# Optimization experiments

Measured on AMD Instinct MI355X. Metric: run time of the kernel, lower is better.

The kernel has to match this reference:

```python
import jax, jax.numpy as jnp
import numpy as np

B, C, N = 8, 768, 256
H = 12            # num_heads[0]
D = C // H        # head_dim = 64


def setup_inputs() -> dict:
    key = jax.random.key(0)
    ks = jax.random.split(key, 4)
    s = 0.02
    return {
        "x_ori": jax.random.normal(ks[0], (B, C, N), jnp.float32),
        "cross": jax.random.normal(ks[1], (B, C, N), jnp.float32),
        "W_proj": jax.random.normal(ks[2], (C, C), jnp.float32) * s,
        "b_proj": jnp.zeros((C,), jnp.float32),
        "W_dep": jax.random.normal(ks[3], (C, C), jnp.float32) * s,
        "b_dep": jnp.zeros((C,), jnp.float32),
    }


def reference(x_ori, cross, W_proj, b_proj, W_dep, b_dep):
    # x_ori, cross: [B, C, N] with channel axis factored as (head_dim D, num_heads H)
    Bn, Cn, Nn = x_ori.shape
    Nc = cross.shape[-1]
    scale = D ** (-0.5)

    # 'B (d H) N -> B d (H N)'
    x = x_ori.reshape(Bn, D, H, Nn).reshape(Bn, D, H * Nn)

    # proj over channel axis (1x1 conv): [B, C, Nc]
    cp = jnp.einsum('oc,bcn->bon', W_proj, cross) + b_proj[None, :, None]
    cp = cp.reshape(Bn, D, H, Nc).reshape(Bn, D, H * Nc)      # 'B (d H) Nc -> B d (H Nc)'

    # 'B (d H) Nc -> B (H Nc) d'
    cr = cross.reshape(Bn, D, H, Nc).transpose(0, 2, 3, 1).reshape(Bn, H * Nc, D)

    # raw attention (no softmax in original source)
    atten = jnp.einsum('bdm,bdn->bmn', x, cp) * scale          # [B, H*N, H*Nc]
    out = jnp.einsum('bmn,bnd->bmd', atten, cr)                # [B, H*N, D]

    # 'B (N H) d -> B N (H d)'  (note (num, head) grouping per source)
    out = out.reshape(Bn, Nn, H, D).reshape(Bn, Nn, H * D)

    y = out @ W_dep.T + b_dep                                  # deproj: [B, N, C]
    # skip connection (dropout is identity at eval / drop_ratio=0)
    return x_ori + y.transpose(0, 2, 1)
```

## Files before the change

### kernel.cpp

```cpp
#include <hip/hip_runtime.h>

typedef unsigned short u16;
typedef short bf16x8 __attribute__((ext_vector_type(8)));
typedef float f32x4 __attribute__((ext_vector_type(4)));

#define BB 8
#define CC 768
#define NN 256
#define HH 12
#define DD 64
#define BCN 196608
#define SCALE 0.125f
#define LDP 72

__device__ __forceinline__ u16 f2b(float f) {
    union { float f; unsigned int i; } v; v.f = f;
    unsigned int r = v.i + 0x7FFFu + ((v.i >> 16) & 1u);
    return (u16)(r >> 16);
}

#define MFMA8(ASP, BSP, ACC)                                                              \
    _Pragma("unroll")                                                                     \
    for (int kk = 0; kk < 2; ++kk) {                                                      \
        bf16x8 a0 = *reinterpret_cast<bf16x8*>((ASP) + (wm + tx) * LDP + kk * 32 + q * 8);\
        bf16x8 a1 = *reinterpret_cast<bf16x8*>((ASP) + (wm + 16 + tx) * LDP + kk * 32 + q * 8);\
        bf16x8 b0 = *reinterpret_cast<bf16x8*>((BSP) + (wn + tx) * LDP + kk * 32 + q * 8);\
        bf16x8 b1 = *reinterpret_cast<bf16x8*>((BSP) + (wn + 16 + tx) * LDP + kk * 32 + q * 8);\
        ACC[0][0] = __builtin_amdgcn_mfma_f32_16x16x32_bf16(a0, b0, ACC[0][0], 0, 0, 0);  \
        ACC[0][1] = __builtin_amdgcn_mfma_f32_16x16x32_bf16(a0, b1, ACC[0][1], 0, 0, 0);  \
        ACC[1][0] = __builtin_amdgcn_mfma_f32_16x16x32_bf16(a1, b0, ACC[1][0], 0, 0, 0);  \
        ACC[1][1] = __builtin_amdgcn_mfma_f32_16x16x32_bf16(a1, b1, ACC[1][1], 0, 0, 0);  \
    }

__global__ __launch_bounds__(256) void k_pg(
    const float* __restrict__ Wp, const float* __restrict__ cross,
    const float* __restrict__ bp, float* __restrict__ G)
{
    __shared__ __align__(16) u16 As[64 * LDP];
    __shared__ __align__(16) u16 Bs[64 * LDP];
    __shared__ __align__(16) float T[64][68];
    const int h  = blockIdx.x;
    const int n0 = blockIdx.y * 64;
    const int b  = blockIdx.z;
    const int t = threadIdx.x;
    const int lane = t & 63, wave = t >> 6;
    const int q = lane >> 4, tx = lane & 15;
    const int wm = (wave & 1) * 32, wn = (wave >> 1) * 32;
    const int r4 = t >> 2, cq = t & 3;
    const float* crb = cross + b * BCN;
    const float* wrow = Wp + (r4 * HH + h) * CC;

    f32x4 acc[2][2] = {};
    float4 ra[4], rc[4];
    #pragma unroll
    for (int u = 0; u < 4; ++u) {
        const int cl = (cq + 4 * u) * 4;
        ra[u] = *reinterpret_cast<const float4*>(wrow + cl);
        rc[u] = *reinterpret_cast<const float4*>(crb + r4 * NN + n0 + cl);
    }
    for (int it = 0; it < 12; ++it) {
        if (it > 0) __syncthreads();
        {
            u16* dstA = As + r4 * LDP;
            #pragma unroll
            for (int u = 0; u < 4; ++u) {
                const int cl = (cq + 4 * u) * 4;
                ushort4 w; w.x = f2b(ra[u].x); w.y = f2b(ra[u].y);
                w.z = f2b(ra[u].z); w.w = f2b(ra[u].w);
                *reinterpret_cast<ushort4*>(dstA + cl) = w;
                T[r4][cl + 0] = rc[u].x; T[r4][cl + 1] = rc[u].y;
                T[r4][cl + 2] = rc[u].z; T[r4][cl + 3] = rc[u].w;
            }
        }
        if (it < 11) {
            const int c0 = (it + 1) * 64;
            #pragma unroll
            for (int u = 0; u < 4; ++u) {
                const int cl = (cq + 4 * u) * 4;
                ra[u] = *reinterpret_cast<const float4*>(wrow + c0 + cl);
                rc[u] = *reinterpret_cast<const float4*>(crb + (c0 + r4) * NN + n0 + cl);
            }
        }
        __syncthreads();
        {
            const int nn = t >> 2, dq = t & 3;
            u16* dst = Bs + nn * LDP;
            #pragma unroll
            for (int u = 0; u < 4; ++u) {
                const int c4 = (dq + 4 * u) * 4;
                ushort4 w;
                w.x = f2b(T[c4 + 0][nn]); w.y = f2b(T[c4 + 1][nn]);
                w.z = f2b(T[c4 + 2][nn]); w.w = f2b(T[c4 + 3][nn]);
                *reinterpret_cast<ushort4*>(dst + c4) = w;
            }
        }
        __syncthreads();
        MFMA8(As, Bs, acc)
    }
    __syncthreads();
    float4 rg[4];
    #pragma unroll
    for (int u = 0; u < 4; ++u)
        rg[u] = *reinterpret_cast<const float4*>(crb + (r4 * HH + h) * NN + n0 + (cq + 4 * u) * 4);
    #pragma unroll
    for (int i = 0; i < 2; ++i)
        #pragma unroll
        for (int r = 0; r < 4; ++r) {
            const int ddl = wm + i * 16 + q * 4 + r;
            const float bias = bp[ddl * HH + h];
            #pragma unroll
            for (int j = 0; j < 2; ++j)
                As[ddl * LDP + wn + j * 16 + tx] = f2b(acc[i][j][r] + bias);
        }
    {
        u16* dst = Bs + r4 * LDP;
        #pragma unroll
        for (int u = 0; u < 4; ++u) {
            const int cl = (cq + 4 * u) * 4;
            ushort4 w; w.x = f2b(rg[u].x); w.y = f2b(rg[u].y);
            w.z = f2b(rg[u].z); w.w = f2b(rg[u].w);
            *reinterpret_cast<ushort4*>(dst + cl) = w;
        }
    }
    __syncthreads();
    f32x4 g[2][2] = {};
    MFMA8(As, Bs, g)
    float* Gb = G + b * 4096;
    #pragma unroll
    for (int i = 0; i < 2; ++i)
        #pragma unroll
        for (int j = 0; j < 2; ++j)
            #pragma unroll
            for (int r = 0; r < 4; ++r) {
                const int dd = wm + i * 16 + q * 4 + r;
                const int dc = wn + j * 16 + tx;
                atomicAdd(Gb + dc * DD + dd, g[i][j][r] * SCALE);
            }
}

__global__ __launch_bounds__(256) void k_xm(
    const float* __restrict__ x, const float* __restrict__ G, u16* __restrict__ U)
{
    __shared__ __align__(16) u16 As[64 * LDP];
    __shared__ __align__(16) u16 Bs[64 * LDP];
    __shared__ __align__(16) float T[64][68];
    const int m0 = blockIdx.x * 64;
    const int b  = blockIdx.y;
    const int h   = m0 >> 8;
    const int nn0 = m0 & 255;
    const int t = threadIdx.x;
    const int lane = t & 63, wave = t >> 6;
    const int q = lane >> 4, tx = lane & 15;
    const int wm = (wave & 1) * 32, wn = (wave >> 1) * 32;
    const float* xb = x + b * BCN;
    const float* Gb = G + b * 4096;
    f32x4 acc[2][2] = {};
    {
        const int d = t >> 2, fq = t & 3;
        const float* src = xb + (d * HH + h) * NN + nn0;
        #pragma unroll
        for (int u = 0; u < 4; ++u) {
            const int nl = (fq + 4 * u) * 4;
            float4 v = *reinterpret_cast<const float4*>(src + nl);
            T[d][nl + 0] = v.x; T[d][nl + 1] = v.y; T[d][nl + 2] = v.z; T[d][nl + 3] = v.w;
        }
    }
    {
        const int r = t >> 2, cq = t & 3;
        const float* src = Gb + r * DD;
        u16* dst = Bs + r * LDP;
        #pragma unroll
        for (int u = 0; u < 4; ++u) {
            const int cl = (cq + 4 * u) * 4;
            float4 v = *reinterpret_cast<const float4*>(src + cl);
            ushort4 w; w.x = f2b(v.x); w.y = f2b(v.y); w.z = f2b(v.z); w.w = f2b(v.w);
            *reinterpret_cast<ushort4*>(dst + cl) = w;
        }
    }
    __syncthreads();
    {
        const int nn = t >> 2, dq = t & 3;
        u16* dst = As + nn * LDP;
        #pragma unroll
        for (int u = 0; u < 4; ++u) {
            const int d4 = (dq + 4 * u) * 4;
            ushort4 w;
            w.x = f2b(T[d4 + 0][nn]); w.y = f2b(T[d4 + 1][nn]);
            w.z = f2b(T[d4 + 2][nn]); w.w = f2b(T[d4 + 3][nn]);
            *reinterpret_cast<ushort4*>(dst + d4) = w;
        }
    }
    __syncthreads();
    MFMA8(As, Bs, acc)
    u16* Ub = U + b * BCN;
    #pragma unroll
    for (int i = 0; i < 2; ++i)
        #pragma unroll
        for (int j = 0; j < 2; ++j)
            #pragma unroll
            for (int r = 0; r < 4; ++r) {
                const int m  = m0 + wm + i * 16 + q * 4 + r;
                const int dd = wn + j * 16 + tx;
                Ub[m * DD + dd] = f2b(acc[i][j][r]);
            }
}

__global__ __launch_bounds__(256) void k_dep(
    const float* __restrict__ Wd, const u16* __restrict__ U,
    const float* __restrict__ bd, const float* __restrict__ x, float* __restrict__ out)
{
    __shared__ __align__(16) u16 As[2][64 * LDP];
    __shared__ __align__(16) u16 Bs[2][64 * LDP];
    const int n0 = blockIdx.x * 64;
    const int o0 = blockIdx.y * 64;
    const int b  = blockIdx.z;
    const int t = threadIdx.x;
    const int lane = t & 63, wave = t >> 6;
    const int q = lane >> 4, tx = lane & 15;
    const int wm = (wave & 1) * 32, wn = (wave >> 1) * 32;
    const int r4 = t >> 2, cq = t & 3;
    const int r8 = t >> 3, ch = (t & 7) * 8;
    const u16* Ub = U + b * BCN;
    float4 ra[4]; uint4 rb[2];

    auto loadit = [&](int it) {
        const int c0 = it * 64;
        const float* srcA = Wd + (o0 + r4) * CC + c0;
        #pragma unroll
        for (int u = 0; u < 4; ++u)
            ra[u] = *reinterpret_cast<const float4*>(srcA + (cq + 4 * u) * 4);
        rb[0] = *reinterpret_cast<const uint4*>(Ub + (n0 + r8) * CC + c0 + ch);
        rb[1] = *reinterpret_cast<const uint4*>(Ub + (n0 + r8 + 32) * CC + c0 + ch);
    };
    auto storeit = [&](int buf) {
        u16* dst = As[buf] + r4 * LDP;
        #pragma unroll
        for (int u = 0; u < 4; ++u) {
            const int cl = (cq + 4 * u) * 4;
            ushort4 w; w.x = f2b(ra[u].x); w.y = f2b(ra[u].y);
            w.z = f2b(ra[u].z); w.w = f2b(ra[u].w);
            *reinterpret_cast<ushort4*>(dst + cl) = w;
        }
        *reinterpret_cast<uint4*>(Bs[buf] + r8 * LDP + ch) = rb[0];
        *reinterpret_cast<uint4*>(Bs[buf] + (r8 + 32) * LDP + ch) = rb[1];
    };

    f32x4 acc[2][2] = {};
    loadit(0);
    storeit(0);
    #pragma unroll 2
    for (int it = 0; it < 12; ++it) {
        const int cur = it & 1;
        if (it < 11) loadit(it + 1);
        __syncthreads();
        MFMA8(As[cur], Bs[cur], acc)
        if (it < 11) storeit(cur ^ 1);
    }
    #pragma unroll
    for (int i = 0; i < 2; ++i)
        #pragma unroll
        for (int j = 0; j < 2; ++j)
            #pragma unroll
            for (int r = 0; r < 4; ++r) {
                const int o = o0 + wm + i * 16 + q * 4 + r;
                const int n = n0 + wn + j * 16 + tx;
                const int idx = b * BCN + o * NN + n;
                out[idx] = acc[i][j][r] + bd[o] + x[idx];
            }
}

extern "C" void kernel_launch(void* const* d_in, const int* in_sizes, int n_in,
                              void* d_out, int out_size, void* d_ws, size_t ws_size,
                              hipStream_t stream) {
    const float* x_ori = (const float*)d_in[0];
    const float* cross = (const float*)d_in[1];
    const float* Wp    = (const float*)d_in[2];
    const float* bp    = (const float*)d_in[3];
    const float* Wd    = (const float*)d_in[4];
    const float* bd    = (const float*)d_in[5];
    float* out = (float*)d_out;

    u16*   U  = (u16*)d_ws;
    float* G  = (float*)((char*)d_ws + (size_t)BB * BCN * sizeof(u16));

    hipMemsetAsync(G, 0, (size_t)BB * DD * DD * sizeof(float), stream);
    k_pg <<<dim3(HH, 4, BB), 256, 0, stream>>>(Wp, cross, bp, G);
    k_xm <<<dim3(48, BB), 256, 0, stream>>>(x_ori, G, U);
    k_dep<<<dim3(4, 12, BB), 256, 0, stream>>>(Wd, U, bd, x_ori, out);
}
```

Baseline: 133.3 us.

## Fuse three kernels and memset into one cooperative kernel with grid syncs

Merges the projection/Gram, x-times-G, and deprojection kernels, plus the G zeroing memset, into a single cooperative launch of 384 blocks separated by grid-wide barriers. Shared memory is aliased across the phases. The aim is to remove the memset and the separate kernel launch gaps. In exchange it adds three grid.sync barriers and the overhead of a cooperative launch, and the grid must fit on the device all at once.

```diff
diff --git a/kernel.cpp b/kernel.cpp
--- a/kernel.cpp
+++ b/kernel.cpp
@@ -1,4 +1,7 @@
 #include <hip/hip_runtime.h>
+#include <hip/hip_cooperative_groups.h>
+
+namespace cg = cooperative_groups;
 
 typedef unsigned short u16;
 typedef short bf16x8 __attribute__((ext_vector_type(8)));
@@ -12,6 +15,7 @@
 #define BCN 196608
 #define SCALE 0.125f
 #define LDP 72
+#define BUFB 9216
 
 __device__ __forceinline__ u16 f2b(float f) {
     union { float f; unsigned int i; } v; v.f = f;
@@ -32,241 +36,248 @@
         ACC[1][1] = __builtin_amdgcn_mfma_f32_16x16x32_bf16(a1, b1, ACC[1][1], 0, 0, 0);  \
     }
 
-__global__ __launch_bounds__(256) void k_pg(
+__global__ __launch_bounds__(256, 2) void k_all(
     const float* __restrict__ Wp, const float* __restrict__ cross,
-    const float* __restrict__ bp, float* __restrict__ G)
+    const float* __restrict__ bp, const float* __restrict__ x,
+    const float* __restrict__ Wd, const float* __restrict__ bd,
+    u16* __restrict__ U, float* __restrict__ G, float* __restrict__ out)
 {
-    __shared__ __align__(16) u16 As[64 * LDP];
-    __shared__ __align__(16) u16 Bs[64 * LDP];
-    __shared__ __align__(16) float T[64][68];
-    const int h  = blockIdx.x;
-    const int n0 = blockIdx.y * 64;
-    const int b  = blockIdx.z;
+    __shared__ __align__(16) unsigned char smem[4 * BUFB];
+    cg::grid_group grid = cg::this_grid();
+
+    const int bid = blockIdx.x;
     const int t = threadIdx.x;
     const int lane = t & 63, wave = t >> 6;
     const int q = lane >> 4, tx = lane & 15;
     const int wm = (wave & 1) * 32, wn = (wave >> 1) * 32;
     const int r4 = t >> 2, cq = t & 3;
-    const float* crb = cross + b * BCN;
-    const float* wrow = Wp + (r4 * HH + h) * CC;
-
-    f32x4 acc[2][2] = {};
-    float4 ra[4], rc[4];
-    #pragma unroll
-    for (int u = 0; u < 4; ++u) {
-        const int cl = (cq + 4 * u) * 4;
-        ra[u] = *reinterpret_cast<const float4*>(wrow + cl);
-        rc[u] = *reinterpret_cast<const float4*>(crb + r4 * NN + n0 + cl);
-    }
-    for (int it = 0; it < 12; ++it) {
-        if (it > 0) __syncthreads();
+    const int b = bid / 48;
+
+    if ((bid % 48) == 0) {
+        float4 z = {0.f, 0.f, 0.f, 0.f};
+        float* Gb = G + b * 4096;
+        #pragma unroll
+        for (int j = 0; j < 4; ++j)
+            *reinterpret_cast<float4*>(Gb + t * 4 + j * 1024) = z;
+    }
+
+    {
+        const int h  = bid % 12;
+        const int n0 = ((bid / 12) % 4) * 64;
+        const float* crb = cross + b * BCN;
+        const float* wrow = Wp + (r4 * HH + h) * CC;
+        u16* Asp = (u16*)smem;
+        u16* Bsp = (u16*)(smem + BUFB);
+        float (*T)[68] = (float (*)[68])(smem + 2 * BUFB);
+
+        f32x4 acc[2][2] = {};
+        float4 ra[4], rc[4];
+        #pragma unroll
+        for (int u = 0; u < 4; ++u) {
+            const int cl = (cq + 4 * u) * 4;
+            ra[u] = *reinterpret_cast<const float4*>(wrow + cl);
+            rc[u] = *reinterpret_cast<const float4*>(crb + r4 * NN + n0 + cl);
+        }
+        for (int it = 0; it < 12; ++it) {
+            if (it > 0) __syncthreads();
+            {
+                u16* dstA = Asp + r4 * LDP;
+                #pragma unroll
+                for (int u = 0; u < 4; ++u) {
+                    const int cl = (cq + 4 * u) * 4;
+                    ushort4 w; w.x = f2b(ra[u].x); w.y = f2b(ra[u].y);
+                    w.z = f2b(ra[u].z); w.w = f2b(ra[u].w);
+                    *reinterpret_cast<ushort4*>(dstA + cl) = w;
+                    T[r4][cl + 0] = rc[u].x; T[r4][cl + 1] = rc[u].y;
+                    T[r4][cl + 2] = rc[u].z; T[r4][cl + 3] = rc[u].w;
+                }
+            }
+            if (it < 11) {
+                const int c0 = (it + 1) * 64;
+                #pragma unroll
+                for (int u = 0; u < 4; ++u) {
+                    const int cl = (cq + 4 * u) * 4;
+                    ra[u] = *reinterpret_cast<const float4*>(wrow + c0 + cl);
+                    rc[u] = *reinterpret_cast<const float4*>(crb + (c0 + r4) * NN + n0 + cl);
+                }
+            }
+            __syncthreads();
+            {
+                const int nn = t >> 2, dq = t & 3;
+                u16* dst = Bsp + nn * LDP;
+                #pragma unroll
+                for (int u = 0; u < 4; ++u) {
+                    const int c4 = (dq + 4 * u) * 4;
+                    ushort4 w;
+                    w.x = f2b(T[c4 + 0][nn]); w.y = f2b(T[c4 + 1][nn]);
+                    w.z = f2b(T[c4 + 2][nn]); w.w = f2b(T[c4 + 3][nn]);
+                    *reinterpret_cast<ushort4*>(dst + c4) = w;
+                }
+            }
+            __syncthreads();
+            MFMA8(Asp, Bsp, acc)
+        }
+        __syncthreads();
+        float4 rg[4];
+        #pragma unroll
+        for (int u = 0; u < 4; ++u)
+            rg[u] = *reinterpret_cast<const float4*>(crb + (r4 * HH + h) * NN + n0 + (cq + 4 * u) * 4);
+        #pragma unroll
+        for (int i = 0; i < 2; ++i)
+            #pragma unroll
+            for (int r = 0; r < 4; ++r) {
+                const int ddl = wm + i * 16 + q * 4 + r;
+                const float bias = bp[ddl * HH + h];
+                #pragma unroll
+                for (int j = 0; j < 2; ++j)
+                    Asp[ddl * LDP + wn + j * 16 + tx] = f2b(acc[i][j][r] + bias);
+            }
         {
-            u16* dstA = As + r4 * LDP;
+            u16* dst = Bsp + r4 * LDP;
+            #pragma unroll
+            for (int u = 0; u < 4; ++u) {
+                const int cl = (cq + 4 * u) * 4;
+                ushort4 w; w.x = f2b(rg[u].x); w.y = f2b(rg[u].y);
+                w.z = f2b(rg[u].z); w.w = f2b(rg[u].w);
+                *reinterpret_cast<ushort4*>(dst + cl) = w;
+            }
+        }
+        __syncthreads();
+        f32x4 g[2][2] = {};
+        MFMA8(Asp, Bsp, g)
+
+        grid.sync();
+
+        float* Gb = G + b * 4096;
+        #pragma unroll
+        for (int i = 0; i < 2; ++i)
+            #pragma unroll
+            for (int j = 0; j < 2; ++j)
+                #pragma unroll
+                for (int r = 0; r < 4; ++r) {
+                    const int dd = wm + i * 16 + q * 4 + r;
+                    const int dc = wn + j * 16 + tx;
+                    atomicAdd(Gb + dc * DD + dd, g[i][j][r] * SCALE);
+                }
+    }
+
+    grid.sync();
+
+    {
+        const int m0 = (bid % 48) * 64;
+        const int h = m0 >> 8, nn0 = m0 & 255;
+        const float* xb = x + b * BCN;
+        const float* Gb = G + b * 4096;
+        u16* Asp = (u16*)smem;
+        u16* Bsp = (u16*)(smem + BUFB);
+        float (*T)[68] = (float (*)[68])(smem + 2 * BUFB);
+        f32x4 acc[2][2] = {};
+        {
+            const float* src = xb + (r4 * HH + h) * NN + nn0;
+            #pragma unroll
+            for (int u = 0; u < 4; ++u) {
+                const int nl = (cq + 4 * u) * 4;
+                float4 v = *reinterpret_cast<const float4*>(src + nl);
+                T[r4][nl + 0] = v.x; T[r4][nl + 1] = v.y;
+                T[r4][nl + 2] = v.z; T[r4][nl + 3] = v.w;
+            }
+        }
+        {
+            const float* src = Gb + r4 * DD;
+            u16* dst = Bsp + r4 * LDP;
+            #pragma unroll
+            for (int u = 0; u < 4; ++u) {
+                const int cl = (cq + 4 * u) * 4;
+                float4 v = *reinterpret_cast<const float4*>(src + cl);
+                ushort4 w; w.x = f2b(v.x); w.y = f2b(v.y); w.z = f2b(v.z); w.w = f2b(v.w);
+                *reinterpret_cast<ushort4*>(dst + cl) = w;
+            }
+        }
+        __syncthreads();
+        {
+            const int nn = t >> 2, dq = t & 3;
+            u16* dst = Asp + nn * LDP;
+            #pragma unroll
+            for (int u = 0; u < 4; ++u) {
+                const int d4 = (dq + 4 * u) * 4;
+                ushort4 w;
+                w.x = f2b(T[d4 + 0][nn]); w.y = f2b(T[d4 + 1][nn]);
+                w.z = f2b(T[d4 + 2][nn]); w.w = f2b(T[d4 + 3][nn]);
+                *reinterpret_cast<ushort4*>(dst + d4) = w;
+            }
+        }
+        __syncthreads();
+        MFMA8(Asp, Bsp, acc)
+        u16* Ub = U + b * BCN;
+        #pragma unroll
+        for (int i = 0; i < 2; ++i)
+            #pragma unroll
+            for (int j = 0; j < 2; ++j)
+                #pragma unroll
+                for (int r = 0; r < 4; ++r) {
+                    const int m  = m0 + wm + i * 16 + q * 4 + r;
+                    const int dd = wn + j * 16 + tx;
+                    Ub[m * DD + dd] = f2b(acc[i][j][r]);
+                }
+    }
+
+    grid.sync();
+
+    {
+        const int n0 = (bid % 4) * 64;
+        const int o0 = ((bid / 4) % 12) * 64;
+        const int r8 = t >> 3, ch = (t & 7) * 8;
+        const u16* Ub = U + b * BCN;
+        float4 ra[4]; uint4 rb[2];
+
+        auto loadit = [&](int it) {
+            const int c0 = it * 64;
+            const float* srcA = Wd + (o0 + r4) * CC + c0;
+            #pragma unroll
+            for (int u = 0; u < 4; ++u)
+                ra[u] = *reinterpret_cast<const float4*>(srcA + (cq + 4 * u) * 4);
+            rb[0] = *reinterpret_cast<const uint4*>(Ub + (n0 + r8) * CC + c0 + ch);
+            rb[1] = *reinterpret_cast<const uint4*>(Ub + (n0 + r8 + 32) * CC + c0 + ch);
+        };
+        auto storeit = [&](int buf) {
+            u16* dstA = (u16*)(smem + buf * BUFB) + r4 * LDP;
             #pragma unroll
             for (int u = 0; u < 4; ++u) {
                 const int cl = (cq + 4 * u) * 4;
                 ushort4 w; w.x = f2b(ra[u].x); w.y = f2b(ra[u].y);
                 w.z = f2b(ra[u].z); w.w = f2b(ra[u].w);
                 *reinterpret_cast<ushort4*>(dstA + cl) = w;
-                T[r4][cl + 0] = rc[u].x; T[r4][cl + 1] = rc[u].y;
-                T[r4][cl + 2] = rc[u].z; T[r4][cl + 3] = rc[u].w;
-            }
-        }
-        if (it < 11) {
-            const int c0 = (it + 1) * 64;
-            #pragma unroll
-            for (int u = 0; u < 4; ++u) {
-                const int cl = (cq + 4 * u) * 4;
-                ra[u] = *reinterpret_cast<const float4*>(wrow + c0 + cl);
-                rc[u] = *reinterpret_cast<const float4*>(crb + (c0 + r4) * NN + n0 + cl);
-            }
-        }
-        __syncthreads();
-        {
-            const int nn = t >> 2, dq = t & 3;
-            u16* dst = Bs + nn * LDP;
-            #pragma unroll
-            for (int u = 0; u < 4; ++u) {
-                const int c4 = (dq + 4 * u) * 4;
-                ushort4 w;
-                w.x = f2b(T[c4 + 0][nn]); w.y = f2b(T[c4 + 1][nn]);
-                w.z = f2b(T[c4 + 2][nn]); w.w = f2b(T[c4 + 3][nn]);
-                *reinterpret_cast<ushort4*>(dst + c4) = w;
-            }
-        }
-        __syncthreads();
-        MFMA8(As, Bs, acc)
-    }
-    __syncthreads();
-    float4 rg[4];
-    #pragma unroll
-    for (int u = 0; u < 4; ++u)
-        rg[u] = *reinterpret_cast<const float4*>(crb + (r4 * HH + h) * NN + n0 + (cq + 4 * u) * 4);
-    #pragma unroll
-    for (int i = 0; i < 2; ++i)
-        #pragma unroll
-        for (int r = 0; r < 4; ++r) {
-            const int ddl = wm + i * 16 + q * 4 + r;
-            const float bias = bp[ddl * HH + h];
+            }
+            u16* dstB = (u16*)(smem + 2 * BUFB + buf * BUFB);
+            *reinterpret_cast<uint4*>(dstB + r8 * LDP + ch) = rb[0];
+            *reinterpret_cast<uint4*>(dstB + (r8 + 32) * LDP + ch) = rb[1];
+        };
+
+        f32x4 acc[2][2] = {};
+        loadit(0);
+        storeit(0);
+        #pragma unroll 2
+        for (int it = 0; it < 12; ++it) {
+            const int cur = it & 1;
+            if (it < 11) loadit(it + 1);
+            __syncthreads();
+            u16* Asp = (u16*)(smem + cur * BUFB);
+            u16* Bsp = (u16*)(smem + 2 * BUFB + cur * BUFB);
+            MFMA8(Asp, Bsp, acc)
+            if (it < 11) storeit(cur ^ 1);
+        }
+        #pragma unroll
+        for (int i = 0; i < 2; ++i)
             #pragma unroll
             for (int j = 0; j < 2; ++j)
-                As[ddl * LDP + wn + j * 16 + tx] = f2b(acc[i][j][r] + bias);
-        }
-    {
-        u16* dst = Bs + r4 * LDP;
-        #pragma unroll
-        for (int u = 0; u < 4; ++u) {
-            const int cl = (cq + 4 * u) * 4;
-            ushort4 w; w.x = f2b(rg[u].x); w.y = f2b(rg[u].y);
-            w.z = f2b(rg[u].z); w.w = f2b(rg[u].w);
-            *reinterpret_cast<ushort4*>(dst + cl) = w;
-        }
-    }
-    __syncthreads();
-    f32x4 g[2][2] = {};
-    MFMA8(As, Bs, g)
-    float* Gb = G + b * 4096;
-    #pragma unroll
-    for (int i = 0; i < 2; ++i)
-        #pragma unroll
-        for (int j = 0; j < 2; ++j)
-            #pragma unroll
-            for (int r = 0; r < 4; ++r) {
-                const int dd = wm + i * 16 + q * 4 + r;
-                const int dc = wn + j * 16 + tx;
-                atomicAdd(Gb + dc * DD + dd, g[i][j][r] * SCALE);
-            }
-}
-
-__global__ __launch_bounds__(256) void k_xm(
-    const float* __restrict__ x, const float* __restrict__ G, u16* __restrict__ U)
-{
-    __shared__ __align__(16) u16 As[64 * LDP];
-    __shared__ __align__(16) u16 Bs[64 * LDP];
-    __shared__ __align__(16) float T[64][68];
-    const int m0 = blockIdx.x * 64;
-    const int b  = blockIdx.y;
-    const int h   = m0 >> 8;
-    const int nn0 = m0 & 255;
-    const int t = threadIdx.x;
-    const int lane = t & 63, wave = t >> 6;
-    const int q = lane >> 4, tx = lane & 15;
-    const int wm = (wave & 1) * 32, wn = (wave >> 1) * 32;
-    const float* xb = x + b * BCN;
-    const float* Gb = G + b * 4096;
-    f32x4 acc[2][2] = {};
-    {
-        const int d = t >> 2, fq = t & 3;
-        const float* src = xb + (d * HH + h) * NN + nn0;
-        #pragma unroll
-        for (int u = 0; u < 4; ++u) {
-            const int nl = (fq + 4 * u) * 4;
-            float4 v = *reinterpret_cast<const float4*>(src + nl);
-            T[d][nl + 0] = v.x; T[d][nl + 1] = v.y; T[d][nl + 2] = v.z; T[d][nl + 3] = v.w;
-        }
-    }
-    {
-        const int r = t >> 2, cq = t & 3;
-        const float* src = Gb + r * DD;
-        u16* dst = Bs + r * LDP;
-        #pragma unroll
-        for (int u = 0; u < 4; ++u) {
-            const int cl = (cq + 4 * u) * 4;
-            float4 v = *reinterpret_cast<const float4*>(src + cl);
-            ushort4 w; w.x = f2b(v.x); w.y = f2b(v.y); w.z = f2b(v.z); w.w = f2b(v.w);
-            *reinterpret_cast<ushort4*>(dst + cl) = w;
-        }
-    }
-    __syncthreads();
-    {
-        const int nn = t >> 2, dq = t & 3;
-        u16* dst = As + nn * LDP;
-        #pragma unroll
-        for (int u = 0; u < 4; ++u) {
-            const int d4 = (dq + 4 * u) * 4;
-            ushort4 w;
-            w.x = f2b(T[d4 + 0][nn]); w.y = f2b(T[d4 + 1][nn]);
-            w.z = f2b(T[d4 + 2][nn]); w.w = f2b(T[d4 + 3][nn]);
-            *reinterpret_cast<ushort4*>(dst + d4) = w;
-        }
-    }
-    __syncthreads();
-    MFMA8(As, Bs, acc)
-    u16* Ub = U + b * BCN;
-    #pragma unroll
-    for (int i = 0; i < 2; ++i)
-        #pragma unroll
-        for (int j = 0; j < 2; ++j)
-            #pragma unroll
-            for (int r = 0; r < 4; ++r) {
-                const int m  = m0 + wm + i * 16 + q * 4 + r;
-                const int dd = wn + j * 16 + tx;
-                Ub[m * DD + dd] = f2b(acc[i][j][r]);
-            }
-}
-
-__global__ __launch_bounds__(256) void k_dep(
-    const float* __restrict__ Wd, const u16* __restrict__ U,
-    const float* __restrict__ bd, const float* __restrict__ x, float* __restrict__ out)
-{
-    __shared__ __align__(16) u16 As[2][64 * LDP];
-    __shared__ __align__(16) u16 Bs[2][64 * LDP];
-    const int n0 = blockIdx.x * 64;
-    const int o0 = blockIdx.y * 64;
-    const int b  = blockIdx.z;
-    const int t = threadIdx.x;
-    const int lane = t & 63, wave = t >> 6;
-    const int q = lane >> 4, tx = lane & 15;
-    const int wm = (wave & 1) * 32, wn = (wave >> 1) * 32;
-    const int r4 = t >> 2, cq = t & 3;
-    const int r8 = t >> 3, ch = (t & 7) * 8;
-    const u16* Ub = U + b * BCN;
-    float4 ra[4]; uint4 rb[2];
-
-    auto loadit = [&](int it) {
-        const int c0 = it * 64;
-        const float* srcA = Wd + (o0 + r4) * CC + c0;
-        #pragma unroll
-        for (int u = 0; u < 4; ++u)
-            ra[u] = *reinterpret_cast<const float4*>(srcA + (cq + 4 * u) * 4);
-        rb[0] = *reinterpret_cast<const uint4*>(Ub + (n0 + r8) * CC + c0 + ch);
-        rb[1] = *reinterpret_cast<const uint4*>(Ub + (n0 + r8 + 32) * CC + c0 + ch);
-    };
-    auto storeit = [&](int buf) {
-        u16* dst = As[buf] + r4 * LDP;
-        #pragma unroll
-        for (int u = 0; u < 4; ++u) {
-            const int cl = (cq + 4 * u) * 4;
-            ushort4 w; w.x = f2b(ra[u].x); w.y = f2b(ra[u].y);
-            w.z = f2b(ra[u].z); w.w = f2b(ra[u].w);
-            *reinterpret_cast<ushort4*>(dst + cl) = w;
-        }
-        *reinterpret_cast<uint4*>(Bs[buf] + r8 * LDP + ch) = rb[0];
-        *reinterpret_cast<uint4*>(Bs[buf] + (r8 + 32) * LDP + ch) = rb[1];
-    };
-
-    f32x4 acc[2][2] = {};
-    loadit(0);
-    storeit(0);
-    #pragma unroll 2
-    for (int it = 0; it < 12; ++it) {
-        const int cur = it & 1;
-        if (it < 11) loadit(it + 1);
-        __syncthreads();
-        MFMA8(As[cur], Bs[cur], acc)
-        if (it < 11) storeit(cur ^ 1);
-    }
-    #pragma unroll
-    for (int i = 0; i < 2; ++i)
-        #pragma unroll
-        for (int j = 0; j < 2; ++j)
-            #pragma unroll
-            for (int r = 0; r < 4; ++r) {
-                const int o = o0 + wm + i * 16 + q * 4 + r;
-                const int n = n0 + wn + j * 16 + tx;
-                const int idx = b * BCN + o * NN + n;
-                out[idx] = acc[i][j][r] + bd[o] + x[idx];
-            }
+                #pragma unroll
+                for (int r = 0; r < 4; ++r) {
+                    const int o = o0 + wm + i * 16 + q * 4 + r;
+                    const int n = n0 + wn + j * 16 + tx;
+                    const int idx = b * BCN + o * NN + n;
+                    out[idx] = acc[i][j][r] + bd[o] + x[idx];
+                }
+    }
 }
 
 extern "C" void kernel_launch(void* const* d_in, const int* in_sizes, int n_in,
@@ -280,11 +291,11 @@
     const float* bd    = (const float*)d_in[5];
     float* out = (float*)d_out;
 
-    u16*   U  = (u16*)d_ws;
-    float* G  = (float*)((char*)d_ws + (size_t)BB * BCN * sizeof(u16));
-
-    hipMemsetAsync(G, 0, (size_t)BB * DD * DD * sizeof(float), stream);
-    k_pg <<<dim3(HH, 4, BB), 256, 0, stream>>>(Wp, cross, bp, G);
-    k_xm <<<dim3(48, BB), 256, 0, stream>>>(x_ori, G, U);
-    k_dep<<<dim3(4, 12, BB), 256, 0, stream>>>(Wd, U, bd, x_ori, out);
+    u16*   U = (u16*)d_ws;
+    float* G = (float*)((char*)d_ws + (size_t)BB * BCN * sizeof(u16));
+
+    void* args[] = {(void*)&Wp, (void*)&cross, (void*)&bp, (void*)&x_ori,
+                    (void*)&Wd, (void*)&bd, (void*)&U, (void*)&G, (void*)&out};
+    hipLaunchCooperativeKernel(reinterpret_cast<void*>(k_all), dim3(384), dim3(256),
+                               args, 0, stream);
 }
```

New measurement: 269.7 us. 2.02x slower.

## Split projection and gram into separate kernels, fold G zeroing into projection

Applied to the files above, without the earlier changes.

The fused projection+gram kernel is split in two. k_proj computes the full channel projection tile by tile, writes it as bf16 to workspace and zeroes G in place of the memset. k_gram then computes per-batch 64x64 Gram partials over 64-wide K slices of the flattened (H*N) axis and accumulates them with atomics. k_dep also drops its double-buffered LDS pipeline for single-buffered register prefetch. This removes the per-head redundant projection layout and the memset launch, in exchange for an extra kernel launch and a bf16 round trip of the projection through global memory.

```diff
diff --git a/kernel.cpp b/kernel.cpp
--- a/kernel.cpp
+++ b/kernel.cpp
@@ -9,6 +9,7 @@
 #define NN 256
 #define HH 12
 #define DD 64
+#define K3 3072
 #define BCN 196608
 #define SCALE 0.125f
 #define LDP 72
@@ -32,30 +33,39 @@
         ACC[1][1] = __builtin_amdgcn_mfma_f32_16x16x32_bf16(a1, b1, ACC[1][1], 0, 0, 0);  \
     }
 
-__global__ __launch_bounds__(256) void k_pg(
+__global__ __launch_bounds__(256) void k_proj(
     const float* __restrict__ Wp, const float* __restrict__ cross,
-    const float* __restrict__ bp, float* __restrict__ G)
+    const float* __restrict__ bp, u16* __restrict__ cp, float* __restrict__ G)
 {
     __shared__ __align__(16) u16 As[64 * LDP];
     __shared__ __align__(16) u16 Bs[64 * LDP];
     __shared__ __align__(16) float T[64][68];
-    const int h  = blockIdx.x;
-    const int n0 = blockIdx.y * 64;
+    const int n0 = blockIdx.x * 64;
+    const int o0 = blockIdx.y * 64;
     const int b  = blockIdx.z;
     const int t = threadIdx.x;
     const int lane = t & 63, wave = t >> 6;
     const int q = lane >> 4, tx = lane & 15;
     const int wm = (wave & 1) * 32, wn = (wave >> 1) * 32;
     const int r4 = t >> 2, cq = t & 3;
+
+    if (blockIdx.x == 0 && blockIdx.y == 0) {
+        float4 z = {0.f, 0.f, 0.f, 0.f};
+        float* Gb = G + b * 4096;
+        #pragma unroll
+        for (int j = 0; j < 4; ++j)
+            *reinterpret_cast<float4*>(Gb + t * 4 + j * 1024) = z;
+    }
+
     const float* crb = cross + b * BCN;
-    const float* wrow = Wp + (r4 * HH + h) * CC;
+    const float* wsrc = Wp + (o0 + r4) * CC;
 
     f32x4 acc[2][2] = {};
     float4 ra[4], rc[4];
     #pragma unroll
     for (int u = 0; u < 4; ++u) {
         const int cl = (cq + 4 * u) * 4;
-        ra[u] = *reinterpret_cast<const float4*>(wrow + cl);
+        ra[u] = *reinterpret_cast<const float4*>(wsrc + cl);
         rc[u] = *reinterpret_cast<const float4*>(crb + r4 * NN + n0 + cl);
     }
     for (int it = 0; it < 12; ++it) {
@@ -77,7 +87,7 @@
             #pragma unroll
             for (int u = 0; u < 4; ++u) {
                 const int cl = (cq + 4 * u) * 4;
-                ra[u] = *reinterpret_cast<const float4*>(wrow + c0 + cl);
+                ra[u] = *reinterpret_cast<const float4*>(wsrc + c0 + cl);
                 rc[u] = *reinterpret_cast<const float4*>(crb + (c0 + r4) * NN + n0 + cl);
             }
         }
@@ -97,34 +107,54 @@
         __syncthreads();
         MFMA8(As, Bs, acc)
     }
-    __syncthreads();
-    float4 rg[4];
-    #pragma unroll
-    for (int u = 0; u < 4; ++u)
-        rg[u] = *reinterpret_cast<const float4*>(crb + (r4 * HH + h) * NN + n0 + (cq + 4 * u) * 4);
+    u16* cpb = cp + b * BCN;
     #pragma unroll
     for (int i = 0; i < 2; ++i)
         #pragma unroll
-        for (int r = 0; r < 4; ++r) {
-            const int ddl = wm + i * 16 + q * 4 + r;
-            const float bias = bp[ddl * HH + h];
-            #pragma unroll
-            for (int j = 0; j < 2; ++j)
-                As[ddl * LDP + wn + j * 16 + tx] = f2b(acc[i][j][r] + bias);
-        }
-    {
-        u16* dst = Bs + r4 * LDP;
+        for (int j = 0; j < 2; ++j)
+            #pragma unroll
+            for (int r = 0; r < 4; ++r) {
+                const int o = o0 + wm + i * 16 + q * 4 + r;
+                const int n = n0 + wn + j * 16 + tx;
+                cpb[o * NN + n] = f2b(acc[i][j][r] + bp[o]);
+            }
+}
+
+__global__ __launch_bounds__(256) void k_gram(
+    const float* __restrict__ cross, const u16* __restrict__ cp, float* __restrict__ G)
+{
+    __shared__ __align__(16) u16 As[64 * LDP];
+    __shared__ __align__(16) u16 Bs[64 * LDP];
+    const int kb = blockIdx.x * 64;
+    const int b  = blockIdx.y;
+    const int t = threadIdx.x;
+    const int lane = t & 63, wave = t >> 6;
+    const int q = lane >> 4, tx = lane & 15;
+    const int wm = (wave & 1) * 32, wn = (wave >> 1) * 32;
+    const float* crb = cross + b * BCN;
+    const u16* cpb = cp + b * BCN;
+    f32x4 acc[2][2] = {};
+    {
+        const int r = t >> 2, cq = t & 3;
+        const float* src = crb + r * K3 + kb;
+        u16* dst = As + r * LDP;
         #pragma unroll
         for (int u = 0; u < 4; ++u) {
             const int cl = (cq + 4 * u) * 4;
-            ushort4 w; w.x = f2b(rg[u].x); w.y = f2b(rg[u].y);
-            w.z = f2b(rg[u].z); w.w = f2b(rg[u].w);
+            float4 v = *reinterpret_cast<const float4*>(src + cl);
+            ushort4 w; w.x = f2b(v.x); w.y = f2b(v.y); w.z = f2b(v.z); w.w = f2b(v.w);
             *reinterpret_cast<ushort4*>(dst + cl) = w;
         }
     }
+    {
+        const int r = t >> 3, ch = (t & 7) * 8;
+        *reinterpret_cast<uint4*>(Bs + r * LDP + ch) =
+            *reinterpret_cast<const uint4*>(cpb + r * K3 + kb + ch);
+        *reinterpret_cast<uint4*>(Bs + (r + 32) * LDP + ch) =
+            *reinterpret_cast<const uint4*>(cpb + (r + 32) * K3 + kb + ch);
+    }
     __syncthreads();
-    f32x4 g[2][2] = {};
-    MFMA8(As, Bs, g)
+    MFMA8(As, Bs, acc)
     float* Gb = G + b * 4096;
     #pragma unroll
     for (int i = 0; i < 2; ++i)
@@ -133,8 +163,8 @@
             #pragma unroll
             for (int r = 0; r < 4; ++r) {
                 const int dd = wm + i * 16 + q * 4 + r;
-                const int dc = wn + j * 16 + tx;
-                atomicAdd(Gb + dc * DD + dd, g[i][j][r] * SCALE);
+                const int d  = wn + j * 16 + tx;
+                atomicAdd(Gb + dd * DD + d, acc[i][j][r] * SCALE);
             }
 }
 
@@ -209,8 +239,8 @@
     const float* __restrict__ Wd, const u16* __restrict__ U,
     const float* __restrict__ bd, const float* __restrict__ x, float* __restrict__ out)
 {
-    __shared__ __align__(16) u16 As[2][64 * LDP];
-    __shared__ __align__(16) u16 Bs[2][64 * LDP];
+    __shared__ __align__(16) u16 As[64 * LDP];
+    __shared__ __align__(16) u16 Bs[64 * LDP];
     const int n0 = blockIdx.x * 64;
     const int o0 = blockIdx.y * 64;
     const int b  = blockIdx.z;
@@ -221,40 +251,40 @@
     const int r4 = t >> 2, cq = t & 3;
     const int r8 = t >> 3, ch = (t & 7) * 8;
     const u16* Ub = U + b * BCN;
+    const float* srcA0 = Wd + (o0 + r4) * CC;
+
     float4 ra[4]; uint4 rb[2];
-
-    auto loadit = [&](int it) {
-        const int c0 = it * 64;
-        const float* srcA = Wd + (o0 + r4) * CC + c0;
-        #pragma unroll
-        for (int u = 0; u < 4; ++u)
-            ra[u] = *reinterpret_cast<const float4*>(srcA + (cq + 4 * u) * 4);
-        rb[0] = *reinterpret_cast<const uint4*>(Ub + (n0 + r8) * CC + c0 + ch);
-        rb[1] = *reinterpret_cast<const uint4*>(Ub + (n0 + r8 + 32) * CC + c0 + ch);
-    };
-    auto storeit = [&](int buf) {
-        u16* dst = As[buf] + r4 * LDP;
-        #pragma unroll
-        for (int u = 0; u < 4; ++u) {
-            const int cl = (cq + 4 * u) * 4;
-            ushort4 w; w.x = f2b(ra[u].x); w.y = f2b(ra[u].y);
-            w.z = f2b(ra[u].z); w.w = f2b(ra[u].w);
-            *reinterpret_cast<ushort4*>(dst + cl) = w;
-        }
-        *reinterpret_cast<uint4*>(Bs[buf] + r8 * LDP + ch) = rb[0];
-        *reinterpret_cast<uint4*>(Bs[buf] + (r8 + 32) * LDP + ch) = rb[1];
-    };
+    #pragma unroll
+    for (int u = 0; u < 4; ++u)
+        ra[u] = *reinterpret_cast<const float4*>(srcA0 + (cq + 4 * u) * 4);
+    rb[0] = *reinterpret_cast<const uint4*>(Ub + (n0 + r8) * CC + ch);
+    rb[1] = *reinterpret_cast<const uint4*>(Ub + (n0 + r8 + 32) * CC + ch);
 
     f32x4 acc[2][2] = {};
-    loadit(0);
-    storeit(0);
-    #pragma unroll 2
     for (int it = 0; it < 12; ++it) {
-        const int cur = it & 1;
-        if (it < 11) loadit(it + 1);
+        if (it > 0) __syncthreads();
+        {
+            u16* dst = As + r4 * LDP;
+            #pragma unroll
+            for (int u = 0; u < 4; ++u) {
+                const int cl = (cq + 4 * u) * 4;
+                ushort4 w; w.x = f2b(ra[u].x); w.y = f2b(ra[u].y);
+                w.z = f2b(ra[u].z); w.w = f2b(ra[u].w);
+                *reinterpret_cast<ushort4*>(dst + cl) = w;
+            }
+            *reinterpret_cast<uint4*>(Bs + r8 * LDP + ch) = rb[0];
+            *reinterpret_cast<uint4*>(Bs + (r8 + 32) * LDP + ch) = rb[1];
+        }
+        if (it < 11) {
+            const int c0 = (it + 1) * 64;
+            #pragma unroll
+            for (int u = 0; u < 4; ++u)
+                ra[u] = *reinterpret_cast<const float4*>(srcA0 + c0 + (cq + 4 * u) * 4);
+            rb[0] = *reinterpret_cast<const uint4*>(Ub + (n0 + r8) * CC + c0 + ch);
+            rb[1] = *reinterpret_cast<const uint4*>(Ub + (n0 + r8 + 32) * CC + c0 + ch);
+        }
         __syncthreads();
-        MFMA8(As[cur], Bs[cur], acc)
-        if (it < 11) storeit(cur ^ 1);
+        MFMA8(As, Bs, acc)
     }
     #pragma unroll
     for (int i = 0; i < 2; ++i)
@@ -280,11 +310,12 @@
     const float* bd    = (const float*)d_in[5];
     float* out = (float*)d_out;
 
+    u16*   cp = (u16*)d_ws;
     u16*   U  = (u16*)d_ws;
     float* G  = (float*)((char*)d_ws + (size_t)BB * BCN * sizeof(u16));
 
-    hipMemsetAsync(G, 0, (size_t)BB * DD * DD * sizeof(float), stream);
-    k_pg <<<dim3(HH, 4, BB), 256, 0, stream>>>(Wp, cross, bp, G);
-    k_xm <<<dim3(48, BB), 256, 0, stream>>>(x_ori, G, U);
-    k_dep<<<dim3(4, 12, BB), 256, 0, stream>>>(Wd, U, bd, x_ori, out);
-}
+    k_proj<<<dim3(4, 12, BB), 256, 0, stream>>>(Wp, cross, bp, cp, G);
+    k_gram<<<dim3(48, BB), 256, 0, stream>>>(cross, cp, G);
+    k_xm  <<<dim3(48, BB), 256, 0, stream>>>(x_ori, G, U);
+    k_dep <<<dim3(4, 12, BB), 256, 0, stream>>>(Wd, U, bd, x_ori, out);
+}
```

Result: faster. 118.2 us (median of 2 runs) (-11.3%).
